# Optimization experiments

Hardware: AMD Instinct MI355X
Metric: run time of the kernel (lower is better)

The kernel has to match this reference:

```python
import jax, jax.numpy as jnp
import numpy as np

B = 8192
D = 512          # encode_length
H = 1024         # projection hidden
S = 4096         # fine_Nums (fine prototypes)
Y = 256          # coarse_num
GUMBEL_TEMP = 0.5
EPS_LOG = 1e-9
EPS_GUMBEL = 1e-20


def setup_inputs() -> dict:
    key = jax.random.key(0)
    ks = jax.random.split(key, 16)
    g = lambda k, shape, s: jax.random.normal(k, shape, dtype=jnp.float32) * s
    glorot = lambda k, shape: jax.random.uniform(k, shape, dtype=jnp.float32,
                                                 minval=-1.0, maxval=1.0) * jnp.sqrt(6.0 / (shape[0] + shape[1]))
    return {
        "X": jax.random.normal(ks[0], (B, D), dtype=jnp.float32),
        # projectionHead: Linear(D,H) -> ReLU -> Linear(H,D)
        "W1": g(ks[1], (D, H), 0.05), "b1": jnp.zeros((H,), jnp.float32),
        "W2": g(ks[2], (H, D), 0.05), "b2": jnp.zeros((D,), jnp.float32),
        # sigma_head: Linear(D,H) -> ReLU -> Linear(H,D)
        "Ws1": g(ks[3], (D, H), 0.05), "bs1": jnp.zeros((H,), jnp.float32),
        "Ws2": g(ks[4], (H, D), 0.05), "bs2": jnp.zeros((D,), jnp.float32),
        # prototype codebooks (glorot)
        "mu_y": glorot(ks[5], (Y, D)),
        "mu_s": glorot(ks[6], (S, D)),
        # reparameterization + gumbel noise (explicit for determinism)
        "eps": jax.random.normal(ks[7], (B, D), dtype=jnp.float32),
        "u_s": jax.random.uniform(ks[8], (B, S), dtype=jnp.float32),
        "u_y": jax.random.uniform(ks[9], (B, Y), dtype=jnp.float32),
    }


def _neg_sq_dist(x, c):
    # -||x_i - c_j||^2 computed via expansion (same math as (x-c)**2 sum)
    return -(jnp.sum(x * x, -1, keepdims=True)
             - 2.0 * x @ c.T
             + jnp.sum(c * c, -1)[None, :])


def _gumbel_softmax_soft(logits_original, u, temp):
    # torch: logits = log(softmax(logits_original) + 1e-9); y = softmax((logits + g)/temp)
    logits = jnp.log(jax.nn.softmax(logits_original, axis=-1) + EPS_LOG)
    gnoise = -jnp.log(-jnp.log(u + EPS_GUMBEL) + EPS_GUMBEL)
    return jax.nn.softmax((logits + gnoise) / temp, axis=-1)


def reference(X, W1, b1, W2, b2, Ws1, bs1, Ws2, bs2, mu_y, mu_s, eps, u_s, u_y):
    # VAE encode with reparameterization
    mu = jax.nn.relu(X @ W1 + b1) @ W2 + b2                    # [B, D]
    sigma = jax.nn.softplus(jax.nn.relu(X @ Ws1 + bs1) @ Ws2 + bs2)
    Z = mu + sigma * eps                                       # [B, D]

    # fine prototype routing: cdist + gumbel-softmax + hard assign
    logits_s = _neg_sq_dist(Z, mu_s)                            # [B, S]
    soft_prob = _gumbel_softmax_soft(logits_s, u_s, GUMBEL_TEMP)
    fine_idx = jnp.argmax(soft_prob, axis=1)                    # [B]
    hard_prob = jax.nn.one_hot(fine_idx, S, dtype=jnp.float32)  # [B, S]
    z_q = hard_prob @ mu_s                                      # selected fine proto [B, D]

    # coarse routing conditioned on Z and selected fine prototype
    logits_coarse = 0.5 * (_neg_sq_dist(Z, mu_y) + _neg_sq_dist(z_q, mu_y))  # [B, Y]
    soft_prob_y = _gumbel_softmax_soft(logits_coarse, u_y, GUMBEL_TEMP)
    batch_y = jnp.argmax(soft_prob_y, axis=1)                   # [B] int

    return mu, Z, soft_prob, soft_prob_y, hard_prob, batch_y
```

## Files before the change

### kernel.cpp

```cpp
#include <hip/hip_runtime.h>
#include <hip/hip_bf16.h>

#define B_ 8192
#define D_ 512
#define H_ 1024
#define S_ 4096
#define Y_ 256

constexpr size_t O_MU    = 0;
constexpr size_t O_Z     = (size_t)B_ * D_;
constexpr size_t O_SOFT  = O_Z + (size_t)B_ * D_;
constexpr size_t O_SOFTY = O_SOFT + (size_t)B_ * S_;
constexpr size_t O_HARD  = O_SOFTY + (size_t)B_ * Y_;
constexpr size_t O_BY    = O_HARD + (size_t)B_ * S_;

typedef _Float16 half8 __attribute__((ext_vector_type(8)));
typedef float f32x4 __attribute__((ext_vector_type(4)));
typedef unsigned int u32;

__device__ __forceinline__ void gload16(const void* g, void* l) {
  __builtin_amdgcn_global_load_lds((const __attribute__((address_space(1))) u32*)g,
                                   (__attribute__((address_space(3))) u32*)l,
                                   16, 0, 0);
}

__device__ __forceinline__ void split2(float x, _Float16& h, _Float16& l) {
  _Float16 hi = (_Float16)x;
  h = hi;
  l = (_Float16)((x - (float)hi) * 2048.0f);
}

__device__ __forceinline__ float blockMax(float v, float* sh) {
#pragma unroll
  for (int o = 32; o; o >>= 1) v = fmaxf(v, __shfl_xor(v, o));
  if ((threadIdx.x & 63) == 0) sh[threadIdx.x >> 6] = v;
  __syncthreads();
  float r = fmaxf(fmaxf(sh[0], sh[1]), fmaxf(sh[2], sh[3]));
  __syncthreads();
  return r;
}

__device__ __forceinline__ float blockSum(float v, float* sh) {
#pragma unroll
  for (int o = 32; o; o >>= 1) v += __shfl_xor(v, o);
  if ((threadIdx.x & 63) == 0) sh[threadIdx.x >> 6] = v;
  __syncthreads();
  float r = (sh[0] + sh[1]) + (sh[2] + sh[3]);
  __syncthreads();
  return r;
}

__device__ __forceinline__ void blockArgmax(float& v, int& i, float* shf, int* shi) {
#pragma unroll
  for (int o = 32; o; o >>= 1) {
    float v2 = __shfl_xor(v, o);
    int   i2 = __shfl_xor(i, o);
    if (v2 > v || (v2 == v && i2 < i)) { v = v2; i = i2; }
  }
  if ((threadIdx.x & 63) == 0) { shf[threadIdx.x >> 6] = v; shi[threadIdx.x >> 6] = i; }
  __syncthreads();
  float bv = shf[0]; int bi = shi[0];
#pragma unroll
  for (int k = 1; k < 4; ++k) {
    float v2 = shf[k]; int i2 = shi[k];
    if (v2 > bv || (v2 == bv && i2 < bi)) { bv = v2; bi = i2; }
  }
  v = bv; i = bi;
  __syncthreads();
}

__global__ void split_kernel(const float* __restrict__ s, size_t n,
                             _Float16* __restrict__ h, _Float16* __restrict__ l) {
  size_t i = (size_t)blockIdx.x * blockDim.x + threadIdx.x;
  size_t st = (size_t)gridDim.x * blockDim.x;
  for (; i < n; i += st) {
    _Float16 hi, lo;
    split2(s[i], hi, lo);
    h[i] = hi; l[i] = lo;
  }
}

__global__ void tsplit_kernel(const float* __restrict__ W, int K, int N,
                              _Float16* __restrict__ th, _Float16* __restrict__ tl) {
  __shared__ float tile[32][33];
  int nb = blockIdx.x * 32, kb = blockIdx.y * 32;
  int tx = threadIdx.x, ty = threadIdx.y;
  for (int r = ty; r < 32; r += 8)
    tile[r][tx] = W[(size_t)(kb + r) * N + nb + tx];
  __syncthreads();
  for (int r = ty; r < 32; r += 8) {
    float x = tile[tx][r];
    size_t o = (size_t)(nb + r) * K + kb + tx;
    _Float16 hi, lo; split2(x, hi, lo);
    th[o] = hi; tl[o] = lo;
  }
}

__global__ void rownorm_kernel(const float* __restrict__ A, int rows, int K,
                               float* __restrict__ out) {
  int w = threadIdx.x >> 6, lane = threadIdx.x & 63;
  int row = blockIdx.x * 4 + w;
  if (row >= rows) return;
  const float* a = A + (size_t)row * K;
  float s = 0.f;
  for (int k = lane; k < K; k += 64) { float x = a[k]; s += x * x; }
#pragma unroll
  for (int o = 32; o; o >>= 1) s += __shfl_xor(s, o);
  if (lane == 0) out[row] = s;
}

template <int EPI>
__launch_bounds__(256, 2)
__global__ void gemm_split(const _Float16* __restrict__ Ah, const _Float16* __restrict__ Al,
                           const _Float16* __restrict__ Bh, const _Float16* __restrict__ Bl,
                           int N, int K, int lda, int ldc,
                           const float* __restrict__ bias, const float* __restrict__ bias2,
                           float* __restrict__ Cf,
                           _Float16* __restrict__ Ch, _Float16* __restrict__ Cl,
                           const float* __restrict__ rown, const float* __restrict__ coln) {
  __shared__ _Float16 lds[4 * 8192];
  const int tid = threadIdx.x;
  const int w = tid >> 6, lane = tid & 63;
  const int m0 = blockIdx.y * 128, n0 = blockIdx.x * 128;
  const int g4 = lane >> 4, l15 = lane & 15;
  const int ln3 = lane >> 3, l7 = lane & 7;
  const int wsx = l7 ^ ln3;
  const int strideA = (w < 2) ? lda : K;
  const size_t laneoff = (size_t)ln3 * strideA + (size_t)wsx * 8;

  const _Float16* stage_src =
      (w == 0) ? (Ah + (size_t)m0 * lda) :
      (w == 1) ? (Al + (size_t)m0 * lda) :
      (w == 2) ? (Bh + (size_t)n0 * K) : (Bl + (size_t)n0 * K);
  _Float16* stage_dst = &lds[w * 8192];

  const int wm = w >> 1, wn = w & 1;

  f32x4 acc[4][4] = {};
  f32x4 accc[4][4] = {};

  for (int k0 = 0; k0 < K; k0 += 64) {
    const _Float16* sp = stage_src + k0 + laneoff;
#pragma unroll
    for (int q = 0; q < 16; ++q)
      gload16(sp + (size_t)q * 8 * strideA, stage_dst + q * 512);
    __syncthreads();

#pragma unroll
    for (int kk = 0; kk < 2; ++kk) {
      half8 ah[4], al[4], bh[4], bl[4];
#pragma unroll
      for (int mi = 0; mi < 4; ++mi) {
        int row = wm * 64 + mi * 16 + l15;
        int off = row * 64 + (((kk * 4 + g4) ^ (l15 & 7)) * 8);
        ah[mi] = *(const half8*)&lds[off];
        al[mi] = *(const half8*)&lds[8192 + off];
      }
#pragma unroll
      for (int ni = 0; ni < 4; ++ni) {
        int row = wn * 64 + ni * 16 + l15;
        int off = row * 64 + (((kk * 4 + g4) ^ (l15 & 7)) * 8);
        bh[ni] = *(const half8*)&lds[16384 + off];
        bl[ni] = *(const half8*)&lds[24576 + off];
      }
#pragma unroll
      for (int mi = 0; mi < 4; ++mi)
#pragma unroll
        for (int ni = 0; ni < 4; ++ni) {
          acc[mi][ni]  = __builtin_amdgcn_mfma_f32_16x16x32_f16(ah[mi], bh[ni], acc[mi][ni], 0, 0, 0);
          accc[mi][ni] = __builtin_amdgcn_mfma_f32_16x16x32_f16(ah[mi], bl[ni], accc[mi][ni], 0, 0, 0);
          accc[mi][ni] = __builtin_amdgcn_mfma_f32_16x16x32_f16(al[mi], bh[ni], accc[mi][ni], 0, 0, 0);
        }
    }
    __syncthreads();
  }

#pragma unroll
  for (int mi = 0; mi < 4; ++mi)
#pragma unroll
    for (int ni = 0; ni < 4; ++ni)
#pragma unroll
      for (int r = 0; r < 4; ++r) {
        int m = m0 + wm * 64 + mi * 16 + g4 * 4 + r;
        int n = n0 + wn * 64 + ni * 16 + l15;
        float c = acc[mi][ni][r] + accc[mi][ni][r] * (1.0f / 2048.0f);
        size_t idx = (size_t)m * ldc + n;
        if (EPI == 0) {
          float bv = (n < H_) ? bias[n] : bias2[n - H_];
          c = fmaxf(c + bv, 0.0f);
          _Float16 hi, lo; split2(c, hi, lo);
          Ch[idx] = hi; Cl[idx] = lo;
        } else if (EPI == 1) {
          Cf[idx] = c + bias[n];
        } else {
          Cf[idx] = 2.0f * c - rown[m] - coln[n];
        }
      }
}

__global__ __launch_bounds__(256) void kz_kernel(const float* __restrict__ mu,
                                                 const float* __restrict__ ps,
                                                 const float* __restrict__ eps,
                                                 float* __restrict__ out,
                                                 _Float16* __restrict__ Zh,
                                                 _Float16* __restrict__ Zl,
                                                 float* __restrict__ z2) {
  __shared__ float sh[4];
  int row = blockIdx.x, t = threadIdx.x;
  float s = 0.f;
  for (int j = t; j < D_; j += 256) {
    size_t idx = (size_t)row * D_ + j;
    float m = mu[idx], p = ps[idx], e = eps[idx];
    float sp = fmaxf(p, 0.f) + log1pf(expf(-fabsf(p)));
    float z = m + sp * e;
    out[O_MU + idx] = m;
    out[O_Z + idx] = z;
    _Float16 hi, lo; split2(z, hi, lo);
    Zh[idx] = hi; Zl[idx] = lo;
    s += z * z;
  }
#pragma unroll
  for (int o = 32; o; o >>= 1) s += __shfl_xor(s, o);
  if ((t & 63) == 0) sh[t >> 6] = s;
  __syncthreads();
  if (t == 0) z2[row] = (sh[0] + sh[1]) + (sh[2] + sh[3]);
}

__global__ __launch_bounds__(256) void ks_kernel(const float* __restrict__ logits,
                                                 const float* __restrict__ us,
                                                 float* __restrict__ out,
                                                 int* __restrict__ fidx, int row0) {
  __shared__ float shf[4];
  __shared__ int shi[4];
  int row = row0 + blockIdx.x, t = threadIdx.x;
  const float* l = logits + (size_t)blockIdx.x * S_;
  const float* u = us + (size_t)row * S_;

  float v[16];
  float m1 = -3.4e38f;
#pragma unroll
  for (int k = 0; k < 16; ++k) { v[k] = l[t + k * 256]; m1 = fmaxf(m1, v[k]); }
  m1 = blockMax(m1, shf);
  float s1 = 0.f;
#pragma unroll
  for (int k = 0; k < 16; ++k) { v[k] = expf(v[k] - m1); s1 += v[k]; }
  s1 = blockSum(s1, shf);
  float m2 = -3.4e38f;
#pragma unroll
  for (int k = 0; k < 16; ++k) {
    float p = v[k] / s1 + 1e-9f;
    float uu = u[t + k * 256];
    float g = -logf(-logf(uu + 1e-20f) + 1e-20f);
    v[k] = (logf(p) + g) * 2.0f;
    m2 = fmaxf(m2, v[k]);
  }
  m2 = blockMax(m2, shf);
  float s2 = 0.f;
#pragma unroll
  for (int k = 0; k < 16; ++k) { v[k] = expf(v[k] - m2); s2 += v[k]; }
  s2 = blockSum(s2, shf);
  float bv = -3.4e38f; int bi = 0x7fffffff;
#pragma unroll
  for (int k = 0; k < 16; ++k) {
    float p = v[k] / s2;
    out[O_SOFT + (size_t)row * S_ + t + k * 256] = p;
    if (p > bv) { bv = p; bi = t + k * 256; }
  }
  blockArgmax(bv, bi, shf, shi);
#pragma unroll
  for (int k = 0; k < 16; ++k) {
    int j = t + k * 256;
    out[O_HARD + (size_t)row * S_ + j] = (j == bi) ? 1.0f : 0.0f;
  }
  if (t == 0) fidx[row] = bi;
}

__global__ __launch_bounds__(256) void ky_kernel(const float* __restrict__ lzy,
                                                 const float* __restrict__ lsy,
                                                 const int* __restrict__ fidx,
                                                 const float* __restrict__ uy,
                                                 float* __restrict__ out) {
  __shared__ float shf[4];
  __shared__ int shi[4];
  int row = blockIdx.x, t = threadIdx.x;
  int fi = fidx[row];
  float lc = 0.5f * (lzy[(size_t)row * Y_ + t] + lsy[(size_t)fi * Y_ + t]);
  float m1 = blockMax(lc, shf);
  float e = expf(lc - m1);
  float s1 = blockSum(e, shf);
  float p = e / s1 + 1e-9f;
  float g = -logf(-logf(uy[(size_t)row * Y_ + t] + 1e-20f) + 1e-20f);
  float a = (logf(p) + g) * 2.0f;
  float m2 = blockMax(a, shf);
  float y = expf(a - m2);
  float s2 = blockSum(y, shf);
  float sp = y / s2;
  out[O_SOFTY + (size_t)row * Y_ + t] = sp;
  float bv = sp; int bi = t;
  blockArgmax(bv, bi, shf, shi);
  if (t == 0) out[O_BY + row] = (float)bi;
}

extern "C" void kernel_launch(void* const* d_in, const int* in_sizes, int n_in,
                              void* d_out, int out_size, void* d_ws, size_t ws_size,
                              hipStream_t stream) {
  const float* X    = (const float*)d_in[0];
  const float* W1   = (const float*)d_in[1];
  const float* b1   = (const float*)d_in[2];
  const float* W2   = (const float*)d_in[3];
  const float* b2   = (const float*)d_in[4];
  const float* Ws1  = (const float*)d_in[5];
  const float* bs1  = (const float*)d_in[6];
  const float* Ws2  = (const float*)d_in[7];
  const float* bs2  = (const float*)d_in[8];
  const float* mu_y = (const float*)d_in[9];
  const float* mu_s = (const float*)d_in[10];
  const float* eps  = (const float*)d_in[11];
  const float* u_s  = (const float*)d_in[12];
  const float* u_y  = (const float*)d_in[13];
  float* out = (float*)d_out;

  char* ws = (char*)d_ws;
  _Float16* XH    = (_Float16*)(ws + 0);
  _Float16* XL    = (_Float16*)(ws + 8388608);
  _Float16* W1CH  = (_Float16*)(ws + 16777216);
  _Float16* W1CL  = (_Float16*)(ws + 18874368);
  _Float16* W2TH  = (_Float16*)(ws + 20971520);
  _Float16* W2TL  = (_Float16*)(ws + 22020096);
  _Float16* WS2TH = (_Float16*)(ws + 23068672);
  _Float16* WS2TL = (_Float16*)(ws + 24117248);
  _Float16* H1H   = (_Float16*)(ws + 25165824);
  _Float16* H1L   = (_Float16*)(ws + 58720256);
  float*    MUF   = (float*)  (ws + 92274688);
  float*    PSF   = (float*)  (ws + 109051904);
  float*    LOGH  = (float*)  (ws + 0);
  float*    LZY   = (float*)  (ws + 67108864);
  float*    LSY   = (float*)  (ws + 75497472);
  const size_t RB = 125829120;
  _Float16* MSH  = (_Float16*)(ws + RB + 0);
  _Float16* MSL  = (_Float16*)(ws + RB + 4194304);
  _Float16* MYH  = (_Float16*)(ws + RB + 8388608);
  _Float16* MYL  = (_Float16*)(ws + RB + 8650752);
  _Float16* ZH   = (_Float16*)(ws + RB + 8912896);
  _Float16* ZL   = (_Float16*)(ws + RB + 17301504);
  float*    Z2   = (float*)  (ws + RB + 25690112);
  float*    CS2  = (float*)  (ws + RB + 25722880);
  float*    CY2  = (float*)  (ws + RB + 25739264);
  int*      FIDX = (int*)    (ws + RB + 25743360);
  (void)ws_size; (void)in_sizes; (void)n_in; (void)out_size;

  split_kernel<<<2048, 256, 0, stream>>>(X, (size_t)B_ * D_, XH, XL);
  split_kernel<<<2048, 256, 0, stream>>>(mu_s, (size_t)S_ * D_, MSH, MSL);
  split_kernel<<<512, 256, 0, stream>>>(mu_y, (size_t)Y_ * D_, MYH, MYL);
  tsplit_kernel<<<dim3(H_ / 32, D_ / 32), dim3(32, 8), 0, stream>>>(W1, D_, H_, W1CH, W1CL);
  tsplit_kernel<<<dim3(H_ / 32, D_ / 32), dim3(32, 8), 0, stream>>>(Ws1, D_, H_,
      W1CH + (size_t)H_ * D_, W1CL + (size_t)H_ * D_);
  tsplit_kernel<<<dim3(D_ / 32, H_ / 32), dim3(32, 8), 0, stream>>>(W2, H_, D_, W2TH, W2TL);
  tsplit_kernel<<<dim3(D_ / 32, H_ / 32), dim3(32, 8), 0, stream>>>(Ws2, H_, D_, WS2TH, WS2TL);
  rownorm_kernel<<<S_ / 4, 256, 0, stream>>>(mu_s, S_, D_, CS2);
  rownorm_kernel<<<Y_ / 4, 256, 0, stream>>>(mu_y, Y_, D_, CY2);

  gemm_split<0><<<dim3(2 * H_ / 128, B_ / 128), 256, 0, stream>>>(
      XH, XL, W1CH, W1CL, 2 * H_, D_, D_, 2 * H_,
      b1, bs1, nullptr, H1H, H1L, nullptr, nullptr);

  gemm_split<1><<<dim3(D_ / 128, B_ / 128), 256, 0, stream>>>(
      H1H, H1L, W2TH, W2TL, D_, H_, 2 * H_, D_,
      b2, nullptr, MUF, nullptr, nullptr, nullptr, nullptr);
  gemm_split<1><<<dim3(D_ / 128, B_ / 128), 256, 0, stream>>>(
      H1H + H_, H1L + H_, WS2TH, WS2TL, D_, H_, 2 * H_, D_,
      bs2, nullptr, PSF, nullptr, nullptr, nullptr, nullptr);

  kz_kernel<<<B_, 256, 0, stream>>>(MUF, PSF, eps, out, ZH, ZL, Z2);

  gemm_split<2><<<dim3(S_ / 128, 4096 / 128), 256, 0, stream>>>(
      ZH, ZL, MSH, MSL, S_, D_, D_, S_,
      nullptr, nullptr, LOGH, nullptr, nullptr, Z2, CS2);
  ks_kernel<<<4096, 256, 0, stream>>>(LOGH, u_s, out, FIDX, 0);
  gemm_split<2><<<dim3(S_ / 128, 4096 / 128), 256, 0, stream>>>(
      ZH + (size_t)4096 * D_, ZL + (size_t)4096 * D_, MSH, MSL, S_, D_, D_, S_,
      nullptr, nullptr, LOGH, nullptr, nullptr, Z2 + 4096, CS2);
  ks_kernel<<<4096, 256, 0, stream>>>(LOGH, u_s, out, FIDX, 4096);

  gemm_split<2><<<dim3(Y_ / 128, B_ / 128), 256, 0, stream>>>(
      ZH, ZL, MYH, MYL, Y_, D_, D_, Y_,
      nullptr, nullptr, LZY, nullptr, nullptr, Z2, CY2);
  gemm_split<2><<<dim3(Y_ / 128, S_ / 128), 256, 0, stream>>>(
      MSH, MSL, MYH, MYL, Y_, D_, D_, Y_,
      nullptr, nullptr, LSY, nullptr, nullptr, CS2, CY2);
  ky_kernel<<<B_, 256, 0, stream>>>(LZY, LSY, FIDX, u_y, out);
}
```

Measured before the change: 455.0 us.

## Fuse prep kernels, merge second-layer GEMMs, vectorize softmax row kernel

Replaces nine small preprocessing launches (fp16 hi/lo splits, weight transposes, row norms) with one segmented prep kernel. Merges the mu and sigma second-layer GEMMs into a single launch that picks the A-operand column offset and bias per N-tile, writing one interleaved buffer that kz_kernel reads. Vectorizes the fine gumbel-softmax kernel with float4 loads and stores, contiguous per-thread chunks, reciprocal multiplies and fast __expf. The goal is less launch overhead and better memory throughput, at the cost of slightly different exp rounding that could shift argmax ties.

```diff
diff --git a/kernel.cpp b/kernel.cpp
--- a/kernel.cpp
+++ b/kernel.cpp
@@ -69,51 +69,70 @@
   __syncthreads();
 }
 
-__global__ void split_kernel(const float* __restrict__ s, size_t n,
-                             _Float16* __restrict__ h, _Float16* __restrict__ l) {
-  size_t i = (size_t)blockIdx.x * blockDim.x + threadIdx.x;
-  size_t st = (size_t)gridDim.x * blockDim.x;
-  for (; i < n; i += st) {
-    _Float16 hi, lo;
-    split2(s[i], hi, lo);
-    h[i] = hi; l[i] = lo;
-  }
-}
-
-__global__ void tsplit_kernel(const float* __restrict__ W, int K, int N,
-                              _Float16* __restrict__ th, _Float16* __restrict__ tl) {
-  __shared__ float tile[32][33];
-  int nb = blockIdx.x * 32, kb = blockIdx.y * 32;
-  int tx = threadIdx.x, ty = threadIdx.y;
+__device__ void seg_split(const float* __restrict__ s, _Float16* __restrict__ h,
+                          _Float16* __restrict__ l, size_t n, int b, int nb) {
+  size_t i = (size_t)b * 256 + threadIdx.x;
+  size_t st = (size_t)nb * 256;
+  for (; i < n; i += st) { _Float16 hi, lo; split2(s[i], hi, lo); h[i] = hi; l[i] = lo; }
+}
+
+__device__ void seg_tsplit(const float* __restrict__ W, int K, int N,
+                           _Float16* __restrict__ th, _Float16* __restrict__ tl,
+                           int tile, float (*tl_lds)[33]) {
+  int ntn = N / 32;
+  int nb = (tile % ntn) * 32, kb = (tile / ntn) * 32;
+  int tx = threadIdx.x & 31, ty = threadIdx.x >> 5;
   for (int r = ty; r < 32; r += 8)
-    tile[r][tx] = W[(size_t)(kb + r) * N + nb + tx];
+    tl_lds[r][tx] = W[(size_t)(kb + r) * N + nb + tx];
   __syncthreads();
   for (int r = ty; r < 32; r += 8) {
-    float x = tile[tx][r];
+    float x = tl_lds[tx][r];
     size_t o = (size_t)(nb + r) * K + kb + tx;
     _Float16 hi, lo; split2(x, hi, lo);
     th[o] = hi; tl[o] = lo;
   }
 }
 
-__global__ void rownorm_kernel(const float* __restrict__ A, int rows, int K,
-                               float* __restrict__ out) {
+__device__ void seg_rownorm(const float* __restrict__ A, int K, float* __restrict__ out,
+                            int tile) {
   int w = threadIdx.x >> 6, lane = threadIdx.x & 63;
-  int row = blockIdx.x * 4 + w;
-  if (row >= rows) return;
+  int row = tile * 4 + w;
   const float* a = A + (size_t)row * K;
   float s = 0.f;
   for (int k = lane; k < K; k += 64) { float x = a[k]; s += x * x; }
 #pragma unroll
   for (int o = 32; o; o >>= 1) s += __shfl_xor(s, o);
   if (lane == 0) out[row] = s;
+}
+
+__global__ __launch_bounds__(256) void prep_kernel(
+    const float* __restrict__ X, const float* __restrict__ W1, const float* __restrict__ Ws1,
+    const float* __restrict__ W2, const float* __restrict__ Ws2,
+    const float* __restrict__ mu_s, const float* __restrict__ mu_y,
+    _Float16* XH, _Float16* XL, _Float16* MSH, _Float16* MSL,
+    _Float16* MYH, _Float16* MYL,
+    _Float16* W1CH, _Float16* W1CL, _Float16* W2CH, _Float16* W2CL,
+    float* CS2, float* CY2) {
+  __shared__ float tile[32][33];
+  int b = blockIdx.x;
+  if (b < 512)       seg_split(X,    XH,  XL,  (size_t)B_ * D_, b,        512);
+  else if (b < 768)  seg_split(mu_s, MSH, MSL, (size_t)S_ * D_, b - 512,  256);
+  else if (b < 784)  seg_split(mu_y, MYH, MYL, (size_t)Y_ * D_, b - 768,  16);
+  else if (b < 1296) seg_tsplit(W1,  D_, H_, W1CH, W1CL, b - 784, tile);
+  else if (b < 1808) seg_tsplit(Ws1, D_, H_, W1CH + (size_t)H_ * D_,
+                                W1CL + (size_t)H_ * D_, b - 1296, tile);
+  else if (b < 2320) seg_tsplit(W2,  H_, D_, W2CH, W2CL, b - 1808, tile);
+  else if (b < 2832) seg_tsplit(Ws2, H_, D_, W2CH + (size_t)D_ * H_,
+                                W2CL + (size_t)D_ * H_, b - 2320, tile);
+  else if (b < 3856) seg_rownorm(mu_s, D_, CS2, b - 2832);
+  else               seg_rownorm(mu_y, D_, CY2, b - 3856);
 }
 
 template <int EPI>
 __launch_bounds__(256, 2)
 __global__ void gemm_split(const _Float16* __restrict__ Ah, const _Float16* __restrict__ Al,
                            const _Float16* __restrict__ Bh, const _Float16* __restrict__ Bl,
-                           int N, int K, int lda, int ldc,
+                           int N, int K, int lda, int ldc, int nsplit, int aoff2,
                            const float* __restrict__ bias, const float* __restrict__ bias2,
                            float* __restrict__ Cf,
                            _Float16* __restrict__ Ch, _Float16* __restrict__ Cl,
@@ -127,10 +146,11 @@
   const int wsx = l7 ^ ln3;
   const int strideA = (w < 2) ? lda : K;
   const size_t laneoff = (size_t)ln3 * strideA + (size_t)wsx * 8;
+  const int ashift = (n0 >= nsplit) ? aoff2 : 0;
 
   const _Float16* stage_src =
-      (w == 0) ? (Ah + (size_t)m0 * lda) :
-      (w == 1) ? (Al + (size_t)m0 * lda) :
+      (w == 0) ? (Ah + (size_t)m0 * lda + ashift) :
+      (w == 1) ? (Al + (size_t)m0 * lda + ashift) :
       (w == 2) ? (Bh + (size_t)n0 * K) : (Bl + (size_t)n0 * K);
   _Float16* stage_dst = &lds[w * 8192];
 
@@ -186,20 +206,20 @@
         float c = acc[mi][ni][r] + accc[mi][ni][r] * (1.0f / 2048.0f);
         size_t idx = (size_t)m * ldc + n;
         if (EPI == 0) {
-          float bv = (n < H_) ? bias[n] : bias2[n - H_];
+          float bv = (n < nsplit) ? bias[n] : bias2[n - nsplit];
           c = fmaxf(c + bv, 0.0f);
           _Float16 hi, lo; split2(c, hi, lo);
           Ch[idx] = hi; Cl[idx] = lo;
         } else if (EPI == 1) {
-          Cf[idx] = c + bias[n];
+          float bv = (n < nsplit) ? bias[n] : bias2[n - nsplit];
+          Cf[idx] = c + bv;
         } else {
           Cf[idx] = 2.0f * c - rown[m] - coln[n];
         }
       }
 }
 
-__global__ __launch_bounds__(256) void kz_kernel(const float* __restrict__ mu,
-                                                 const float* __restrict__ ps,
+__global__ __launch_bounds__(256) void kz_kernel(const float* __restrict__ MPS,
                                                  const float* __restrict__ eps,
                                                  float* __restrict__ out,
                                                  _Float16* __restrict__ Zh,
@@ -210,7 +230,9 @@
   float s = 0.f;
   for (int j = t; j < D_; j += 256) {
     size_t idx = (size_t)row * D_ + j;
-    float m = mu[idx], p = ps[idx], e = eps[idx];
+    float m = MPS[(size_t)row * 1024 + j];
+    float p = MPS[(size_t)row * 1024 + 512 + j];
+    float e = eps[idx];
     float sp = fmaxf(p, 0.f) + log1pf(expf(-fabsf(p)));
     float z = m + sp * e;
     out[O_MU + idx] = m;
@@ -233,44 +255,68 @@
   __shared__ float shf[4];
   __shared__ int shi[4];
   int row = row0 + blockIdx.x, t = threadIdx.x;
-  const float* l = logits + (size_t)blockIdx.x * S_;
-  const float* u = us + (size_t)row * S_;
+  const float4* l4 = (const float4*)(logits + (size_t)blockIdx.x * S_) + t * 4;
+  const float4* u4 = (const float4*)(us + (size_t)row * S_) + t * 4;
 
   float v[16];
+#pragma unroll
+  for (int q = 0; q < 4; ++q) {
+    float4 x = l4[q];
+    v[q * 4 + 0] = x.x; v[q * 4 + 1] = x.y; v[q * 4 + 2] = x.z; v[q * 4 + 3] = x.w;
+  }
   float m1 = -3.4e38f;
 #pragma unroll
-  for (int k = 0; k < 16; ++k) { v[k] = l[t + k * 256]; m1 = fmaxf(m1, v[k]); }
+  for (int k = 0; k < 16; ++k) m1 = fmaxf(m1, v[k]);
   m1 = blockMax(m1, shf);
   float s1 = 0.f;
 #pragma unroll
-  for (int k = 0; k < 16; ++k) { v[k] = expf(v[k] - m1); s1 += v[k]; }
+  for (int k = 0; k < 16; ++k) { v[k] = __expf(v[k] - m1); s1 += v[k]; }
   s1 = blockSum(s1, shf);
+  float is1 = 1.0f / s1;
   float m2 = -3.4e38f;
 #pragma unroll
-  for (int k = 0; k < 16; ++k) {
-    float p = v[k] / s1 + 1e-9f;
-    float uu = u[t + k * 256];
-    float g = -logf(-logf(uu + 1e-20f) + 1e-20f);
-    v[k] = (logf(p) + g) * 2.0f;
-    m2 = fmaxf(m2, v[k]);
+  for (int q = 0; q < 4; ++q) {
+    float4 uu = u4[q];
+    float ua[4] = {uu.x, uu.y, uu.z, uu.w};
+#pragma unroll
+    for (int e = 0; e < 4; ++e) {
+      int k = q * 4 + e;
+      float p = v[k] * is1 + 1e-9f;
+      float g = -logf(-logf(ua[e] + 1e-20f) + 1e-20f);
+      v[k] = (logf(p) + g) * 2.0f;
+      m2 = fmaxf(m2, v[k]);
+    }
   }
   m2 = blockMax(m2, shf);
   float s2 = 0.f;
 #pragma unroll
-  for (int k = 0; k < 16; ++k) { v[k] = expf(v[k] - m2); s2 += v[k]; }
+  for (int k = 0; k < 16; ++k) { v[k] = __expf(v[k] - m2); s2 += v[k]; }
   s2 = blockSum(s2, shf);
+  float is2 = 1.0f / s2;
   float bv = -3.4e38f; int bi = 0x7fffffff;
-#pragma unroll
-  for (int k = 0; k < 16; ++k) {
-    float p = v[k] / s2;
-    out[O_SOFT + (size_t)row * S_ + t + k * 256] = p;
-    if (p > bv) { bv = p; bi = t + k * 256; }
+  float* so = out + O_SOFT + (size_t)row * S_ + (size_t)t * 16;
+#pragma unroll
+  for (int q = 0; q < 4; ++q) {
+    float pe[4];
+#pragma unroll
+    for (int e = 0; e < 4; ++e) {
+      int k = q * 4 + e;
+      pe[e] = v[k] * is2;
+      if (pe[e] > bv) { bv = pe[e]; bi = t * 16 + k; }
+    }
+    float4 pv; pv.x = pe[0]; pv.y = pe[1]; pv.z = pe[2]; pv.w = pe[3];
+    ((float4*)so)[q] = pv;
   }
   blockArgmax(bv, bi, shf, shi);
-#pragma unroll
-  for (int k = 0; k < 16; ++k) {
-    int j = t + k * 256;
-    out[O_HARD + (size_t)row * S_ + j] = (j == bi) ? 1.0f : 0.0f;
+  float* ho = out + O_HARD + (size_t)row * S_ + (size_t)t * 16;
+#pragma unroll
+  for (int q = 0; q < 4; ++q) {
+    float4 hv;
+    hv.x = (t * 16 + q * 4 + 0 == bi) ? 1.f : 0.f;
+    hv.y = (t * 16 + q * 4 + 1 == bi) ? 1.f : 0.f;
+    hv.z = (t * 16 + q * 4 + 2 == bi) ? 1.f : 0.f;
+    hv.w = (t * 16 + q * 4 + 3 == bi) ? 1.f : 0.f;
+    ((float4*)ho)[q] = hv;
   }
   if (t == 0) fidx[row] = bi;
 }
@@ -286,13 +332,13 @@
   int fi = fidx[row];
   float lc = 0.5f * (lzy[(size_t)row * Y_ + t] + lsy[(size_t)fi * Y_ + t]);
   float m1 = blockMax(lc, shf);
-  float e = expf(lc - m1);
+  float e = __expf(lc - m1);
   float s1 = blockSum(e, shf);
   float p = e / s1 + 1e-9f;
   float g = -logf(-logf(uy[(size_t)row * Y_ + t] + 1e-20f) + 1e-20f);
   float a = (logf(p) + g) * 2.0f;
   float m2 = blockMax(a, shf);
-  float y = expf(a - m2);
+  float y = __expf(a - m2);
   float s2 = blockSum(y, shf);
   float sp = y / s2;
   out[O_SOFTY + (size_t)row * Y_ + t] = sp;
@@ -325,14 +371,11 @@
   _Float16* XL    = (_Float16*)(ws + 8388608);
   _Float16* W1CH  = (_Float16*)(ws + 16777216);
   _Float16* W1CL  = (_Float16*)(ws + 18874368);
-  _Float16* W2TH  = (_Float16*)(ws + 20971520);
-  _Float16* W2TL  = (_Float16*)(ws + 22020096);
-  _Float16* WS2TH = (_Float16*)(ws + 23068672);
-  _Float16* WS2TL = (_Float16*)(ws + 24117248);
+  _Float16* W2CH  = (_Float16*)(ws + 20971520);
+  _Float16* W2CL  = (_Float16*)(ws + 23068672);
   _Float16* H1H   = (_Float16*)(ws + 25165824);
   _Float16* H1L   = (_Float16*)(ws + 58720256);
-  float*    MUF   = (float*)  (ws + 92274688);
-  float*    PSF   = (float*)  (ws + 109051904);
+  float*    MPS   = (float*)  (ws + 92274688);
   float*    LOGH  = (float*)  (ws + 0);
   float*    LZY   = (float*)  (ws + 67108864);
   float*    LSY   = (float*)  (ws + 75497472);
@@ -349,44 +392,34 @@
   int*      FIDX = (int*)    (ws + RB + 25743360);
   (void)ws_size; (void)in_sizes; (void)n_in; (void)out_size;
 
-  split_kernel<<<2048, 256, 0, stream>>>(X, (size_t)B_ * D_, XH, XL);
-  split_kernel<<<2048, 256, 0, stream>>>(mu_s, (size_t)S_ * D_, MSH, MSL);
-  split_kernel<<<512, 256, 0, stream>>>(mu_y, (size_t)Y_ * D_, MYH, MYL);
-  tsplit_kernel<<<dim3(H_ / 32, D_ / 32), dim3(32, 8), 0, stream>>>(W1, D_, H_, W1CH, W1CL);
-  tsplit_kernel<<<dim3(H_ / 32, D_ / 32), dim3(32, 8), 0, stream>>>(Ws1, D_, H_,
-      W1CH + (size_t)H_ * D_, W1CL + (size_t)H_ * D_);
-  tsplit_kernel<<<dim3(D_ / 32, H_ / 32), dim3(32, 8), 0, stream>>>(W2, H_, D_, W2TH, W2TL);
-  tsplit_kernel<<<dim3(D_ / 32, H_ / 32), dim3(32, 8), 0, stream>>>(Ws2, H_, D_, WS2TH, WS2TL);
-  rownorm_kernel<<<S_ / 4, 256, 0, stream>>>(mu_s, S_, D_, CS2);
-  rownorm_kernel<<<Y_ / 4, 256, 0, stream>>>(mu_y, Y_, D_, CY2);
+  prep_kernel<<<3920, 256, 0, stream>>>(X, W1, Ws1, W2, Ws2, mu_s, mu_y,
+                                        XH, XL, MSH, MSL, MYH, MYL,
+                                        W1CH, W1CL, W2CH, W2CL, CS2, CY2);
 
   gemm_split<0><<<dim3(2 * H_ / 128, B_ / 128), 256, 0, stream>>>(
-      XH, XL, W1CH, W1CL, 2 * H_, D_, D_, 2 * H_,
+      XH, XL, W1CH, W1CL, 2 * H_, D_, D_, 2 * H_, H_, 0,
       b1, bs1, nullptr, H1H, H1L, nullptr, nullptr);
 
-  gemm_split<1><<<dim3(D_ / 128, B_ / 128), 256, 0, stream>>>(
-      H1H, H1L, W2TH, W2TL, D_, H_, 2 * H_, D_,
-      b2, nullptr, MUF, nullptr, nullptr, nullptr, nullptr);
-  gemm_split<1><<<dim3(D_ / 128, B_ / 128), 256, 0, stream>>>(
-      H1H + H_, H1L + H_, WS2TH, WS2TL, D_, H_, 2 * H_, D_,
-      bs2, nullptr, PSF, nullptr, nullptr, nullptr, nullptr);
-
-  kz_kernel<<<B_, 256, 0, stream>>>(MUF, PSF, eps, out, ZH, ZL, Z2);
+  gemm_split<1><<<dim3(2 * D_ / 128, B_ / 128), 256, 0, stream>>>(
+      H1H, H1L, W2CH, W2CL, 2 * D_, H_, 2 * H_, 2 * D_, D_, H_,
+      b2, bs2, MPS, nullptr, nullptr, nullptr, nullptr);
+
+  kz_kernel<<<B_, 256, 0, stream>>>(MPS, eps, out, ZH, ZL, Z2);
 
   gemm_split<2><<<dim3(S_ / 128, 4096 / 128), 256, 0, stream>>>(
-      ZH, ZL, MSH, MSL, S_, D_, D_, S_,
+      ZH, ZL, MSH, MSL, S_, D_, D_, S_, S_, 0,
       nullptr, nullptr, LOGH, nullptr, nullptr, Z2, CS2);
   ks_kernel<<<4096, 256, 0, stream>>>(LOGH, u_s, out, FIDX, 0);
   gemm_split<2><<<dim3(S_ / 128, 4096 / 128), 256, 0, stream>>>(
-      ZH + (size_t)4096 * D_, ZL + (size_t)4096 * D_, MSH, MSL, S_, D_, D_, S_,
+      ZH + (size_t)4096 * D_, ZL + (size_t)4096 * D_, MSH, MSL, S_, D_, D_, S_, S_, 0,
       nullptr, nullptr, LOGH, nullptr, nullptr, Z2 + 4096, CS2);
   ks_kernel<<<4096, 256, 0, stream>>>(LOGH, u_s, out, FIDX, 4096);
 
   gemm_split<2><<<dim3(Y_ / 128, B_ / 128), 256, 0, stream>>>(
-      ZH, ZL, MYH, MYL, Y_, D_, D_, Y_,
+      ZH, ZL, MYH, MYL, Y_, D_, D_, Y_, Y_, 0,
       nullptr, nullptr, LZY, nullptr, nullptr, Z2, CY2);
   gemm_split<2><<<dim3(Y_ / 128, S_ / 128), 256, 0, stream>>>(
-      MSH, MSL, MYH, MYL, Y_, D_, D_, Y_,
+      MSH, MSL, MYH, MYL, Y_, D_, D_, Y_, Y_, 0,
       nullptr, nullptr, LSY, nullptr, nullptr, CS2, CY2);
   ky_kernel<<<B_, 256, 0, stream>>>(LZY, LSY, FIDX, u_y, out);
 }
```

Result: faster. 418.4 us (-8.1%).
